# Kernel optimization log

Hardware: AMD Instinct MI355X
Metric: run time of the kernel (lower is better)

Reference implementation:

```python
import jax, jax.numpy as jnp
import numpy as np

N_NODES = 100000
N_EDGES = 1600000


def _graph_conv(num_nodes, edge_index, feat, w, b, in_feats, out_feats):
    src, dst = edge_index[0], edge_index[1]
    # degree of source endpoints, clamp(min=1)^-0.5
    deg = jax.ops.segment_sum(jnp.ones_like(src, dtype=jnp.float32), src, num_segments=num_nodes)
    norm = jnp.power(jnp.clip(deg, 1.0), -0.5)[:, None]  # [N,1]
    feat = feat * norm
    if in_feats > out_feats:
        feat = feat @ w                                   # [N,out]
        rst = jax.ops.segment_sum(feat[src], dst, num_segments=num_nodes)
    else:
        rst = jax.ops.segment_sum(feat[src], dst, num_segments=num_nodes)
        rst = rst @ w
    rst = rst * norm + b
    return jax.nn.relu(rst)


def setup_inputs() -> dict:
    key = jax.random.key(0)
    ks = jax.random.split(key, 8)
    features = jax.random.normal(ks[0], (N_NODES, 256), dtype=jnp.float32)
    e_subgraph = jax.random.randint(ks[1], (2, N_EDGES), 0, N_NODES, dtype=jnp.int64 if jax.config.jax_enable_x64 else jnp.int32)
    n_subgraph = jnp.zeros((N_NODES,), dtype=jnp.int32)
    to_fetch = jax.random.randint(ks[2], (16,), 0, N_NODES, dtype=jnp.int32)
    # GraphConv weights (xavier-like scale), Linear weight (out,in) per F.linear
    w1 = jax.random.normal(ks[3], (256, 128), dtype=jnp.float32) * (2.0 / (256 + 128)) ** 0.5
    b1 = jnp.zeros((128,), dtype=jnp.float32)
    w2 = jax.random.normal(ks[4], (128, 128), dtype=jnp.float32) * (2.0 / (128 + 128)) ** 0.5
    b2 = jnp.zeros((128,), dtype=jnp.float32)
    w3 = jax.random.normal(ks[5], (16, 128), dtype=jnp.float32) * (2.0 / 128) ** 0.5
    b3 = jnp.zeros((16,), dtype=jnp.float32)
    return {"n_subgraph": n_subgraph, "e_subgraph": e_subgraph, "to_fetch": to_fetch,
            "features": features, "w1": w1, "b1": b1, "w2": w2, "b2": b2, "w3": w3, "b3": b3}


def reference(n_subgraph, e_subgraph, to_fetch, features, w1, b1, w2, b2, w3, b3):
    num_nodes = n_subgraph.shape[0]
    h = features.astype(jnp.float32)
    h = _graph_conv(num_nodes, e_subgraph, h, w1, b1, 256, 128)
    h = _graph_conv(num_nodes, e_subgraph, h, w2, b2, 128, 128)
    h = h @ w3.T + b3  # F.linear
    return (h, h)
```

## Files before the change

### kernel.cpp

```cpp
#include <hip/hip_runtime.h>

#define AP 40
#define H2P 136
#define PB 120
#define NPB 256
#define NBUKMAX 512
#define CAPE 8192

typedef short bf16x8 __attribute__((ext_vector_type(8)));
typedef float f32x4 __attribute__((ext_vector_type(4)));

static __device__ __forceinline__ ushort f2bf(float f) {
  unsigned u = __float_as_uint(f);
  unsigned r = (u + 0x7fffu + ((u >> 16) & 1u)) >> 16;
  return (ushort)r;
}
static __device__ __forceinline__ float bflo(unsigned u) { return __uint_as_float(u << 16); }
static __device__ __forceinline__ float bfhi(unsigned u) { return __uint_as_float(u & 0xffff0000u); }
static __device__ __forceinline__ unsigned packbf(float lo, float hi) {
  return (unsigned)f2bf(lo) | ((unsigned)f2bf(hi) << 16);
}

__global__ __launch_bounds__(256) void k_hist2(const int* __restrict__ src,
                                               const int* __restrict__ dst, int E,
                                               unsigned* __restrict__ planes, int HW,
                                               int* __restrict__ hist) {
  __shared__ unsigned lds[25600];
  __shared__ int cnt[NBUKMAX];
  const int per = (E + PB - 1) / PB;
  const int s0 = blockIdx.x * per;
  const int s1 = min(E, s0 + per);
  for (int i = threadIdx.x; i < HW; i += 256) lds[i] = 0u;
  for (int i = threadIdx.x; i < NBUKMAX; i += 256) cnt[i] = 0;
  __syncthreads();
  for (int j = s0 + threadIdx.x; j < s1; j += 256) {
    int k = src[j];
    atomicAdd(&lds[k >> 2], 1u << ((k & 3) * 8));
    atomicAdd(&cnt[dst[j] >> 8], 1);
  }
  __syncthreads();
  unsigned* out = planes + (size_t)blockIdx.x * HW;
  for (int i = threadIdx.x; i < HW; i += 256) out[i] = lds[i];
  for (int i = threadIdx.x; i < NBUKMAX; i += 256) hist[i * PB + blockIdx.x] = cnt[i];
}

__global__ void k_reduce_cvt(const unsigned* __restrict__ planes, int HW,
                             float* __restrict__ nrm, int N, int nrb,
                             const float* __restrict__ w1, const float* __restrict__ w2,
                             const float* __restrict__ w3, ushort* __restrict__ w1P,
                             ushort* __restrict__ w2T, ushort* __restrict__ w3b,
                             int* __restrict__ hist) {
  __shared__ int s[256];
  if ((int)blockIdx.x < nrb) {
    int w = blockIdx.x * 256 + threadIdx.x;
    if (w >= HW) return;
    const unsigned* base = planes + w;
    unsigned c0 = 0, c1 = 0, c2 = 0, c3 = 0;
    for (int b = 0; b < PB; b++) {
      unsigned u = base[(size_t)b * HW];
      c0 += u & 255u; c1 += (u >> 8) & 255u; c2 += (u >> 16) & 255u; c3 += u >> 24;
    }
    int n0 = w * 4;
    unsigned c[4] = {c0, c1, c2, c3};
#pragma unroll
    for (int j = 0; j < 4; j++)
      if (n0 + j < N) {
        float d = (float)c[j];
        if (d < 1.f) d = 1.f;
        nrm[n0 + j] = 1.f / sqrtf(d);
      }
  } else if ((int)blockIdx.x < nrb + 200) {
    int i = (blockIdx.x - nrb) * 256 + threadIdx.x;
    if (i < 32768) {
      int frag = i >> 9, within = i & 511;
      int lane = within >> 3, e = within & 7;
      int k0s = frag >> 3, ni = frag & 7;
      int row = ni * 16 + (lane & 15);
      int col = k0s * 32 + (lane >> 4) * 8 + e;
      w1P[i] = f2bf(w1[col * 128 + row]);
    } else if (i < 49152) {
      int j = i - 32768;
      int c = j >> 7, k = j & 127;
      w2T[j] = f2bf(w2[k * 128 + c]);
    } else if (i < 51200) {
      int j = i - 49152;
      w3b[j] = f2bf(w3[j]);
    }
  } else {
    int t = threadIdx.x;
    int b0 = t * 2, b1 = t * 2 + 1;
    int tot0 = 0, tot1 = 0;
    for (int blk = 0; blk < PB; blk++) tot0 += hist[b0 * PB + blk];
    for (int blk = 0; blk < PB; blk++) tot1 += hist[b1 * PB + blk];
    int pair = tot0 + tot1;
    s[t] = pair;
    __syncthreads();
    for (int o = 1; o < 256; o <<= 1) {
      int x = (t >= o) ? s[t - o] : 0;
      __syncthreads();
      s[t] += x;
      __syncthreads();
    }
    int base = s[t] - pair;
    for (int blk = 0; blk < PB; blk++) { int v = hist[b0 * PB + blk]; hist[b0 * PB + blk] = base; base += v; }
    for (int blk = 0; blk < PB; blk++) { int v = hist[b1 * PB + blk]; hist[b1 * PB + blk] = base; base += v; }
  }
}

__global__ __launch_bounds__(256) void k_p1_gemm1(const int* __restrict__ src,
                                                  const int* __restrict__ dst, int E,
                                                  const int* __restrict__ hist,
                                                  unsigned* __restrict__ pairs,
                                                  const float* __restrict__ feat,
                                                  const ushort* __restrict__ w1P,
                                                  const float* __restrict__ nrm,
                                                  ushort* __restrict__ Xb, int N) {
  __shared__ int cur[NBUKMAX];
  if ((int)blockIdx.x < PB) {
    for (int i = threadIdx.x; i < NBUKMAX; i += 256) cur[i] = hist[i * PB + blockIdx.x];
    __syncthreads();
    const int per = (E + PB - 1) / PB;
    const int s0 = blockIdx.x * per;
    const int s1 = min(E, s0 + per);
    for (int j = s0 + threadIdx.x; j < s1; j += 256) {
      int d = dst[j];
      int pos = atomicAdd(&cur[d >> 8], 1);
      pairs[pos] = ((unsigned)src[j] << 8) | (unsigned)(d & 255);
    }
    return;
  }
  const int tid = threadIdx.x;
  const int row0 = (blockIdx.x - PB) * 64;
  const int wv = tid >> 6, lane = tid & 63;
  const int rbase = wv * 16;
  const int lr = lane & 15;
  const int kh = (lane >> 4) * 8;

  const int gr = row0 + rbase + lr;
  const bool valid = (gr < N);
  const float* fb = feat + (size_t)gr * 256 + kh;

  f32x4 acc[8];
#pragma unroll
  for (int ni = 0; ni < 8; ni++) acc[ni] = (f32x4)0.f;

#pragma unroll
  for (int ks = 0; ks < 8; ks++) {
    float4 a = make_float4(0.f, 0.f, 0.f, 0.f), b = a;
    if (valid) {
      a = *(const float4*)(fb + ks * 32);
      b = *(const float4*)(fb + ks * 32 + 4);
    }
    union { bf16x8 v; ushort u[8]; } bu;
    bu.u[0] = f2bf(a.x); bu.u[1] = f2bf(a.y); bu.u[2] = f2bf(a.z); bu.u[3] = f2bf(a.w);
    bu.u[4] = f2bf(b.x); bu.u[5] = f2bf(b.y); bu.u[6] = f2bf(b.z); bu.u[7] = f2bf(b.w);
    const ushort* wbase = w1P + (size_t)ks * 8 * 512 + lane * 8;
#pragma unroll
    for (int ni = 0; ni < 8; ni++) {
      bf16x8 afrag = *(const bf16x8*)&wbase[ni * 512];
      acc[ni] = __builtin_amdgcn_mfma_f32_16x16x32_bf16(afrag, bu.v, acc[ni], 0, 0, 0);
    }
  }
  if (valid) {
    float nv = nrm[gr];
#pragma unroll
    for (int ni = 0; ni < 8; ni++) {
      int c0 = ni * 16 + (lane >> 4) * 4;
      ushort4 u;
      u.x = f2bf(acc[ni][0] * nv);
      u.y = f2bf(acc[ni][1] * nv);
      u.z = f2bf(acc[ni][2] * nv);
      u.w = f2bf(acc[ni][3] * nv);
      *(ushort4*)&Xb[(size_t)gr * 128 + c0] = u;
    }
  }
}

__global__ __launch_bounds__(256) void k_p2_place(const unsigned* __restrict__ pairs,
                                                  const int* __restrict__ hist,
                                                  int* __restrict__ csr,
                                                  int* __restrict__ row_start,
                                                  int N, int E) {
  __shared__ int stage[CAPE];
  __shared__ int cnt[NPB];
  __shared__ int scn[NPB];
  const int b = blockIdx.x;
  const int t = threadIdx.x;
  const int n0 = b << 8;
  const int n1 = min(N, n0 + NPB);
  const int nn = n1 - n0;
  const int e0 = hist[b * PB];
  const int e1 = hist[(b + 1) * PB];
  for (int i = t; i < nn; i += 256) cnt[i] = 0;
  __syncthreads();
  for (int j = e0 + t; j < e1; j += 256) atomicAdd(&cnt[pairs[j] & 255u], 1);
  __syncthreads();
  int v = (t < nn) ? cnt[t] : 0;
  scn[t] = v;
  __syncthreads();
  for (int o = 1; o < NPB; o <<= 1) {
    int x = (t >= o) ? scn[t - o] : 0;
    __syncthreads();
    scn[t] += x;
    __syncthreads();
  }
  int excl = scn[t] - v;
  if (t < nn) row_start[n0 + t] = e0 + excl;
  if (t == NPB - 1 && n1 == N) row_start[N] = e0 + scn[t];
  __syncthreads();
  if (t < nn) cnt[t] = excl;
  __syncthreads();
  const int seg = e1 - e0;
  if (seg <= CAPE) {
    for (int j = e0 + t; j < e1; j += 256) {
      unsigned pr = pairs[j];
      int rpos = atomicAdd(&cnt[pr & 255u], 1);
      stage[rpos] = (int)(pr >> 8);
    }
    __syncthreads();
    for (int j = t; j < seg; j += 256) csr[e0 + j] = stage[j];
  } else {
    for (int j = e0 + t; j < e1; j += 256) {
      unsigned pr = pairs[j];
      int rpos = atomicAdd(&cnt[pr & 255u], 1);
      csr[e0 + rpos] = (int)(pr >> 8);
    }
  }
}

__global__ __launch_bounds__(256) void k_agg_bf(const ushort* __restrict__ Xin,
                                                const int* __restrict__ rs,
                                                const int* __restrict__ csr,
                                                const float* __restrict__ nrm,
                                                const float* __restrict__ bias,
                                                ushort* __restrict__ Out, int N, int fused) {
  const int wv = threadIdx.x >> 6, lane = threadIdx.x & 63;
  const int d = blockIdx.x * 4 + wv;
  if (d >= N) return;
  const unsigned* X = (const unsigned*)Xin;
  int s0 = rs[d], s1 = rs[d + 1];
  float a0 = 0.f, a1 = 0.f;
  int j = s0;
  for (; j + 4 <= s1; j += 4) {
    int i0 = csr[j], i1 = csr[j + 1], i2 = csr[j + 2], i3 = csr[j + 3];
    unsigned u0 = X[(size_t)i0 * 64 + lane];
    unsigned u1 = X[(size_t)i1 * 64 + lane];
    unsigned u2 = X[(size_t)i2 * 64 + lane];
    unsigned u3 = X[(size_t)i3 * 64 + lane];
    a0 += (bflo(u0) + bflo(u1)) + (bflo(u2) + bflo(u3));
    a1 += (bfhi(u0) + bfhi(u1)) + (bfhi(u2) + bfhi(u3));
  }
  for (; j < s1; j++) {
    unsigned u = X[(size_t)csr[j] * 64 + lane];
    a0 += bflo(u);
    a1 += bfhi(u);
  }
  unsigned o;
  if (fused) {
    float nv = nrm[d];
    float2 b = *(const float2*)&bias[lane * 2];
    float h0 = fmaxf(a0 * nv + b.x, 0.f) * nv;
    float h1 = fmaxf(a1 * nv + b.y, 0.f) * nv;
    o = packbf(h0, h1);
  } else {
    o = packbf(a0, a1);
  }
  ((unsigned*)Out)[(size_t)d * 64 + lane] = o;
}

__global__ __launch_bounds__(256) void k_gemm23_mfma(const ushort* __restrict__ Agg2,
                                                     const float* __restrict__ nrm,
                                                     const ushort* __restrict__ w2T,
                                                     const float* __restrict__ b2,
                                                     const ushort* __restrict__ w3b,
                                                     const float* __restrict__ b3,
                                                     float* __restrict__ out, int N) {
  __shared__ __align__(16) char lds_raw[128 * H2P * 2];
  ushort* As = (ushort*)lds_raw;
  ushort* Bs = As + 128 * AP;
  ushort* h2s = (ushort*)lds_raw;

  const int tid = threadIdx.x;
  const int row0 = blockIdx.x * 128;
  const int wv = tid >> 6, lane = tid & 63;
  const int rbase = wv * 32;
  const int lr = lane & 15;
  const int kl = (lane >> 4) * 8;

  f32x4 acc[8][2];
#pragma unroll
  for (int ni = 0; ni < 8; ni++)
#pragma unroll
    for (int mi = 0; mi < 2; mi++) acc[ni][mi] = (f32x4)0.f;

  for (int k0 = 0; k0 < 128; k0 += 32) {
    __syncthreads();
#pragma unroll
    for (int j = 0; j < 4; j++) {
      int e = (tid + j * 256) * 4;
      int r = e >> 5, k = e & 31;
      int gr = row0 + r;
      ushort4 v = make_ushort4(0, 0, 0, 0);
      if (gr < N) v = *(const ushort4*)&Agg2[(size_t)gr * 128 + k0 + k];
      *(ushort4*)&As[r * AP + k] = v;
    }
#pragma unroll
    for (int j = 0; j < 4; j++) {
      int e = (tid + j * 256) * 4;
      int c = e >> 5, k = e & 31;
      ushort4 v = *(const ushort4*)&w2T[(size_t)c * 128 + k0 + k];
      *(ushort4*)&Bs[c * AP + k] = v;
    }
    __syncthreads();
    bf16x8 bfrag[2], afrag[8];
#pragma unroll
    for (int mi = 0; mi < 2; mi++)
      bfrag[mi] = *(const bf16x8*)&As[(rbase + mi * 16 + lr) * AP + kl];
#pragma unroll
    for (int ni = 0; ni < 8; ni++)
      afrag[ni] = *(const bf16x8*)&Bs[(ni * 16 + lr) * AP + kl];
#pragma unroll
    for (int ni = 0; ni < 8; ni++)
#pragma unroll
      for (int mi = 0; mi < 2; mi++)
        acc[ni][mi] = __builtin_amdgcn_mfma_f32_16x16x32_bf16(afrag[ni], bfrag[mi], acc[ni][mi], 0, 0, 0);
  }
  __syncthreads();

#pragma unroll
  for (int mi = 0; mi < 2; mi++) {
    int r = rbase + mi * 16 + lr;
    int gr = row0 + r;
    float nv = (gr < N) ? nrm[gr] : 0.f;
#pragma unroll
    for (int ni = 0; ni < 8; ni++) {
      int c0 = ni * 16 + (lane >> 4) * 4;
      float4 bb = *(const float4*)&b2[c0];
      ushort4 u;
      u.x = f2bf(fmaxf(acc[ni][mi][0] * nv + bb.x, 0.f));
      u.y = f2bf(fmaxf(acc[ni][mi][1] * nv + bb.y, 0.f));
      u.z = f2bf(fmaxf(acc[ni][mi][2] * nv + bb.z, 0.f));
      u.w = f2bf(fmaxf(acc[ni][mi][3] * nv + bb.w, 0.f));
      *(ushort4*)&h2s[r * H2P + c0] = u;
    }
  }
  f32x4 acc3[2];
  acc3[0] = (f32x4)0.f;
  acc3[1] = (f32x4)0.f;
#pragma unroll
  for (int ks = 0; ks < 4; ks++) {
    bf16x8 a3 = *(const bf16x8*)&w3b[(size_t)lr * 128 + ks * 32 + kl];
#pragma unroll
    for (int mi = 0; mi < 2; mi++) {
      bf16x8 b3f = *(const bf16x8*)&h2s[(rbase + mi * 16 + lr) * H2P + ks * 32 + kl];
      acc3[mi] = __builtin_amdgcn_mfma_f32_16x16x32_bf16(a3, b3f, acc3[mi], 0, 0, 0);
    }
  }
#pragma unroll
  for (int mi = 0; mi < 2; mi++) {
    int gr = row0 + rbase + mi * 16 + lr;
    if (gr < N) {
      int o0 = (lane >> 4) * 4;
      float4 bb = *(const float4*)&b3[o0];
      float4 v;
      v.x = acc3[mi][0] + bb.x;
      v.y = acc3[mi][1] + bb.y;
      v.z = acc3[mi][2] + bb.z;
      v.w = acc3[mi][3] + bb.w;
      *(float4*)&out[(size_t)gr * 16 + o0] = v;
      *(float4*)&out[(size_t)(N + gr) * 16 + o0] = v;
    }
  }
}

extern "C" void kernel_launch(void* const* d_in, const int* in_sizes, int n_in,
                              void* d_out, int out_size, void* d_ws, size_t ws_size,
                              hipStream_t stream) {
  const int N = in_sizes[0];
  const int E = in_sizes[1] / 2;
  const int HW = (N + 3) / 4;
  const int NBUK = (N + NPB - 1) / NPB;
  const int nrb = (HW + 255) / 256;

  const int* e_sub = (const int*)d_in[1];
  const int* src = e_sub;
  const int* dst = e_sub + E;
  const float* feat = (const float*)d_in[3];
  const float* w1 = (const float*)d_in[4];
  const float* b1 = (const float*)d_in[5];
  const float* w2 = (const float*)d_in[6];
  const float* b2 = (const float*)d_in[7];
  const float* w3 = (const float*)d_in[8];
  const float* b3 = (const float*)d_in[9];
  float* out = (float*)d_out;

  char* p = (char*)d_ws;
  auto alloc = [&](size_t bytes) { void* r = (void*)p; p += (bytes + 255) & ~(size_t)255; return r; };
  int* row_start = (int*)alloc((size_t)(N + 1) * 4);
  int* csr = (int*)alloc((size_t)E * 4);
  int* hist = (int*)alloc((size_t)(NBUKMAX + 1) * PB * 4);
  unsigned* pairs = (unsigned*)alloc((size_t)E * 4);
  float* nrm = (float*)alloc((size_t)N * 4);
  ushort* w1P = (ushort*)alloc((size_t)128 * 256 * 2);
  ushort* w2T = (ushort*)alloc((size_t)128 * 128 * 2);
  ushort* w3b = (ushort*)alloc((size_t)16 * 128 * 2);
  ushort* Xb = (ushort*)alloc((size_t)N * 128 * 2);
  ushort* Hb = (ushort*)alloc((size_t)N * 128 * 2);
  unsigned* planes = (unsigned*)alloc((size_t)PB * HW * 4);

  k_hist2<<<PB, 256, 0, stream>>>(src, dst, E, planes, HW, hist);
  k_reduce_cvt<<<nrb + 201, 256, 0, stream>>>(planes, HW, nrm, N, nrb, w1, w2, w3, w1P, w2T,
                                              w3b, hist);
  k_p1_gemm1<<<PB + (N + 63) / 64, 256, 0, stream>>>(src, dst, E, hist, pairs, feat, w1P,
                                                     nrm, Xb, N);
  k_p2_place<<<NBUK, 256, 0, stream>>>(pairs, hist, csr, row_start, N, E);
  k_agg_bf<<<(N + 3) / 4, 256, 0, stream>>>(Xb, row_start, csr, nrm, b1, Hb, N, 1);
  k_agg_bf<<<(N + 3) / 4, 256, 0, stream>>>(Hb, row_start, csr, nrm, b1, Xb, N, 0);
  k_gemm23_mfma<<<(N + 127) / 128, 256, 0, stream>>>(Xb, nrm, w2T, b2, w3b, b3, out, N);
}
```

Baseline: 287.9 us.

## Split edge scatter from GEMM1 and compute two row tiles per wave

```diff
diff --git a/kernel.cpp b/kernel.cpp
--- a/kernel.cpp
+++ b/kernel.cpp
@@ -107,71 +107,79 @@
   }
 }
 
-__global__ __launch_bounds__(256) void k_p1_gemm1(const int* __restrict__ src,
-                                                  const int* __restrict__ dst, int E,
-                                                  const int* __restrict__ hist,
-                                                  unsigned* __restrict__ pairs,
-                                                  const float* __restrict__ feat,
-                                                  const ushort* __restrict__ w1P,
-                                                  const float* __restrict__ nrm,
-                                                  ushort* __restrict__ Xb, int N) {
+__global__ __launch_bounds__(256) void k_p1_scatter(const int* __restrict__ src,
+                                                    const int* __restrict__ dst, int E,
+                                                    const int* __restrict__ hist,
+                                                    unsigned* __restrict__ pairs) {
   __shared__ int cur[NBUKMAX];
-  if ((int)blockIdx.x < PB) {
-    for (int i = threadIdx.x; i < NBUKMAX; i += 256) cur[i] = hist[i * PB + blockIdx.x];
-    __syncthreads();
-    const int per = (E + PB - 1) / PB;
-    const int s0 = blockIdx.x * per;
-    const int s1 = min(E, s0 + per);
-    for (int j = s0 + threadIdx.x; j < s1; j += 256) {
-      int d = dst[j];
-      int pos = atomicAdd(&cur[d >> 8], 1);
-      pairs[pos] = ((unsigned)src[j] << 8) | (unsigned)(d & 255);
-    }
-    return;
-  }
+  for (int i = threadIdx.x; i < NBUKMAX; i += 256) cur[i] = hist[i * PB + blockIdx.x];
+  __syncthreads();
+  const int per = (E + PB - 1) / PB;
+  const int s0 = blockIdx.x * per;
+  const int s1 = min(E, s0 + per);
+  for (int j = s0 + threadIdx.x; j < s1; j += 256) {
+    int d = dst[j];
+    int pos = atomicAdd(&cur[d >> 8], 1);
+    pairs[pos] = ((unsigned)src[j] << 8) | (unsigned)(d & 255);
+  }
+}
+
+__global__ __launch_bounds__(256) void k_gemm1(const float* __restrict__ feat,
+                                               const ushort* __restrict__ w1P,
+                                               const float* __restrict__ nrm,
+                                               ushort* __restrict__ Xb, int N) {
   const int tid = threadIdx.x;
-  const int row0 = (blockIdx.x - PB) * 64;
+  const int row0 = blockIdx.x * 128;
   const int wv = tid >> 6, lane = tid & 63;
-  const int rbase = wv * 16;
+  const int rbase = wv * 32;
   const int lr = lane & 15;
   const int kh = (lane >> 4) * 8;
 
-  const int gr = row0 + rbase + lr;
-  const bool valid = (gr < N);
-  const float* fb = feat + (size_t)gr * 256 + kh;
-
-  f32x4 acc[8];
-#pragma unroll
-  for (int ni = 0; ni < 8; ni++) acc[ni] = (f32x4)0.f;
+  const int gr0 = row0 + rbase + lr;
+  const int gr1 = gr0 + 16;
+  const bool v0 = (gr0 < N), v1 = (gr1 < N);
+  const float* fb0 = feat + (size_t)gr0 * 256 + kh;
+  const float* fb1 = feat + (size_t)gr1 * 256 + kh;
+
+  f32x4 acc[2][8];
+#pragma unroll
+  for (int mi = 0; mi < 2; mi++)
+#pragma unroll
+    for (int ni = 0; ni < 8; ni++) acc[mi][ni] = (f32x4)0.f;
 
 #pragma unroll
   for (int ks = 0; ks < 8; ks++) {
-    float4 a = make_float4(0.f, 0.f, 0.f, 0.f), b = a;
-    if (valid) {
-      a = *(const float4*)(fb + ks * 32);
-      b = *(const float4*)(fb + ks * 32 + 4);
-    }
-    union { bf16x8 v; ushort u[8]; } bu;
-    bu.u[0] = f2bf(a.x); bu.u[1] = f2bf(a.y); bu.u[2] = f2bf(a.z); bu.u[3] = f2bf(a.w);
-    bu.u[4] = f2bf(b.x); bu.u[5] = f2bf(b.y); bu.u[6] = f2bf(b.z); bu.u[7] = f2bf(b.w);
+    float4 a0 = make_float4(0.f, 0.f, 0.f, 0.f), b0 = a0, a1 = a0, b1 = a0;
+    if (v0) { a0 = *(const float4*)(fb0 + ks * 32); b0 = *(const float4*)(fb0 + ks * 32 + 4); }
+    if (v1) { a1 = *(const float4*)(fb1 + ks * 32); b1 = *(const float4*)(fb1 + ks * 32 + 4); }
+    union { bf16x8 v; ushort u[8]; } f0, f1;
+    f0.u[0] = f2bf(a0.x); f0.u[1] = f2bf(a0.y); f0.u[2] = f2bf(a0.z); f0.u[3] = f2bf(a0.w);
+    f0.u[4] = f2bf(b0.x); f0.u[5] = f2bf(b0.y); f0.u[6] = f2bf(b0.z); f0.u[7] = f2bf(b0.w);
+    f1.u[0] = f2bf(a1.x); f1.u[1] = f2bf(a1.y); f1.u[2] = f2bf(a1.z); f1.u[3] = f2bf(a1.w);
+    f1.u[4] = f2bf(b1.x); f1.u[5] = f2bf(b1.y); f1.u[6] = f2bf(b1.z); f1.u[7] = f2bf(b1.w);
     const ushort* wbase = w1P + (size_t)ks * 8 * 512 + lane * 8;
 #pragma unroll
     for (int ni = 0; ni < 8; ni++) {
       bf16x8 afrag = *(const bf16x8*)&wbase[ni * 512];
-      acc[ni] = __builtin_amdgcn_mfma_f32_16x16x32_bf16(afrag, bu.v, acc[ni], 0, 0, 0);
-    }
-  }
-  if (valid) {
-    float nv = nrm[gr];
-#pragma unroll
-    for (int ni = 0; ni < 8; ni++) {
-      int c0 = ni * 16 + (lane >> 4) * 4;
-      ushort4 u;
-      u.x = f2bf(acc[ni][0] * nv);
-      u.y = f2bf(acc[ni][1] * nv);
-      u.z = f2bf(acc[ni][2] * nv);
-      u.w = f2bf(acc[ni][3] * nv);
-      *(ushort4*)&Xb[(size_t)gr * 128 + c0] = u;
+      acc[0][ni] = __builtin_amdgcn_mfma_f32_16x16x32_bf16(afrag, f0.v, acc[0][ni], 0, 0, 0);
+      acc[1][ni] = __builtin_amdgcn_mfma_f32_16x16x32_bf16(afrag, f1.v, acc[1][ni], 0, 0, 0);
+    }
+  }
+#pragma unroll
+  for (int mi = 0; mi < 2; mi++) {
+    int gr = (mi ? gr1 : gr0);
+    if (gr < N) {
+      float nv = nrm[gr];
+#pragma unroll
+      for (int ni = 0; ni < 8; ni++) {
+        int c0 = ni * 16 + (lane >> 4) * 4;
+        ushort4 u;
+        u.x = f2bf(acc[mi][ni][0] * nv);
+        u.y = f2bf(acc[mi][ni][1] * nv);
+        u.z = f2bf(acc[mi][ni][2] * nv);
+        u.w = f2bf(acc[mi][ni][3] * nv);
+        *(ushort4*)&Xb[(size_t)gr * 128 + c0] = u;
+      }
     }
   }
 }
@@ -411,8 +419,8 @@
   k_hist2<<<PB, 256, 0, stream>>>(src, dst, E, planes, HW, hist);
   k_reduce_cvt<<<nrb + 201, 256, 0, stream>>>(planes, HW, nrm, N, nrb, w1, w2, w3, w1P, w2T,
                                               w3b, hist);
-  k_p1_gemm1<<<PB + (N + 63) / 64, 256, 0, stream>>>(src, dst, E, hist, pairs, feat, w1P,
-                                                     nrm, Xb, N);
+  k_p1_scatter<<<PB, 256, 0, stream>>>(src, dst, E, hist, pairs);
+  k_gemm1<<<(N + 127) / 128, 256, 0, stream>>>(feat, w1P, nrm, Xb, N);
   k_p2_place<<<NBUK, 256, 0, stream>>>(pairs, hist, csr, row_start, N, E);
   k_agg_bf<<<(N + 3) / 4, 256, 0, stream>>>(Xb, row_start, csr, nrm, b1, Hb, N, 1);
   k_agg_bf<<<(N + 3) / 4, 256, 0, stream>>>(Hb, row_start, csr, nrm, b1, Xb, N, 0);
```

New measurement: 314.1 us. +9.1%, slower.
